# Kernel tuning notes

Hardware: AMD Instinct MI355X
Metric: run time of the kernel (lower is better)

Reference implementation:

```python
import jax, jax.numpy as jnp
import numpy as np

N, D, H = 4096, 1024, 8
DH = D // H
EPS = 1e-5


def layer_norm(x, g, b):
    mu = jnp.mean(x, axis=-1, keepdims=True)
    var = jnp.mean(jnp.square(x - mu), axis=-1, keepdims=True)
    return (x - mu) * jax.lax.rsqrt(var + EPS) * g + b


def setup_inputs() -> dict:
    key = jax.random.key(0)
    ks = jax.random.split(key, 12)
    s = 0.02
    inp = {
        "x": jax.random.normal(ks[0], (N, D), dtype=jnp.float32),
        "adj": (jax.random.uniform(ks[1], (N, N)) < 0.01).astype(jnp.float32),
        "Wq": jax.random.normal(ks[2], (D, D), dtype=jnp.float32) * s,
        "Wk": jax.random.normal(ks[3], (D, D), dtype=jnp.float32) * s,
        "Wv": jax.random.normal(ks[4], (D, D), dtype=jnp.float32) * s,
        "Wo_w": jax.random.normal(ks[5], (D, D), dtype=jnp.float32) * s,
        "Wo_b": jnp.zeros((D,), dtype=jnp.float32),
        "adj_bias": jnp.full((H,), 1.0, dtype=jnp.float32),
        "ln1_g": jnp.ones((D,), dtype=jnp.float32),
        "ln1_b": jnp.zeros((D,), dtype=jnp.float32),
        "ffn_ln_g": jnp.ones((D,), dtype=jnp.float32),
        "ffn_ln_b": jnp.zeros((D,), dtype=jnp.float32),
        "ffn_w1": jax.random.normal(ks[6], (D, 2 * D), dtype=jnp.float32) * s,
        "ffn_b1": jnp.zeros((2 * D,), dtype=jnp.float32),
        "ffn_w2": jax.random.normal(ks[7], (2 * D, D), dtype=jnp.float32) * s,
        "ffn_b2": jnp.zeros((D,), dtype=jnp.float32),
    }
    return inp


def reference(x, adj, Wq, Wk, Wv, Wo_w, Wo_b, adj_bias, ln1_g, ln1_b,
              ffn_ln_g, ffn_ln_b, ffn_w1, ffn_b1, ffn_w2, ffn_b2):
    scale = DH ** -0.5
    Q = (x @ Wq).reshape(N, H, DH)
    K = (x @ Wk).reshape(N, H, DH)
    V = (x @ Wv).reshape(N, H, DH)
    # attn[i,h,j] = <Q_i, K_j> * scale + beta_h * adj[i,j]
    attn = jnp.einsum('bhd,nhd->bhn', Q, K) * scale
    attn = attn + adj_bias[None, :, None] * adj[:, None, :]
    attn = jax.nn.softmax(attn, axis=-1)  # dropout in eval mode -> identity
    out = jnp.einsum('bhn,nhd->bhd', attn, V).reshape(N, D)
    out = out @ Wo_w + Wo_b
    h = layer_norm(x + out, ln1_g, ln1_b)
    f = layer_norm(h, ffn_ln_g, ffn_ln_b)
    f = jax.nn.gelu(f @ ffn_w1 + ffn_b1, approximate=False) @ ffn_w2 + ffn_b2
    return h + f
```

## Files before the change

### kernel.cpp

```cpp
#include <hip/hip_runtime.h>
#include <hip/hip_bf16.h>
#include <cstdint>
#include <cstddef>

typedef __hip_bfloat16 bf16;
typedef __attribute__((ext_vector_type(8))) short short8;
typedef __attribute__((ext_vector_type(4))) short short4v;
typedef __attribute__((ext_vector_type(4))) float floatx4;
typedef unsigned long long u64;

#define DEVI static __device__ __forceinline__

DEVI void load_lds16(const void* g, void* l) {
  __builtin_amdgcn_global_load_lds((const __attribute__((address_space(1))) unsigned int*)g,
                                   (__attribute__((address_space(3))) unsigned int*)l, 16, 0, 0);
}
DEVI short8 ld8(const bf16* p) { return *(const short8*)p; }
DEVI floatx4 mfma16(short8 a, short8 b, floatx4 c) {
  return __builtin_amdgcn_mfma_f32_16x16x32_bf16(a, b, c, 0, 0, 0);
}
DEVI short bfb(float f) { bf16 h = __float2bfloat16(f); return __builtin_bit_cast(short, h); }
DEVI float fbf(short s) { bf16 h = __builtin_bit_cast(bf16, s); return __bfloat162float(h); }

DEVI void tr_tile(const float* in, bf16* out, int R, int C, int bx, int by) {
  __shared__ float t[32][33];
  int c0 = bx * 32, r0 = by * 32;
  int tx = threadIdx.x & 31, ty = threadIdx.x >> 5;
#pragma unroll
  for (int i = 0; i < 32; i += 8) t[ty + i][tx] = in[(size_t)(r0 + ty + i) * C + c0 + tx];
  __syncthreads();
#pragma unroll
  for (int i = 0; i < 32; i += 8)
    out[(size_t)(c0 + ty + i) * R + r0 + tx] = __float2bfloat16(t[tx][ty + i]);
}

__global__ __launch_bounds__(256)
void prep_all(const float* __restrict__ x, bf16* __restrict__ xb,
              const float* __restrict__ adj, u64* __restrict__ bits,
              const float* Wq, const float* Wk, const float* Wv, const float* Wo,
              const float* W1, const float* W2,
              bf16* Wqkvt, bf16* Wot, bf16* W1t, bf16* W2t) {
  int id = blockIdx.x;
  if (id < 4096) {
    const int row = id, tid = threadIdx.x;
    const int wave = tid >> 6, lane = tid & 63;
    float4 v = ((const float4*)(x + (size_t)row * 1024))[tid];
    bf16* o = xb + (size_t)row * 1024 + tid * 4;
    o[0] = __float2bfloat16(v.x); o[1] = __float2bfloat16(v.y);
    o[2] = __float2bfloat16(v.z); o[3] = __float2bfloat16(v.w);
    const float* arow = adj + (size_t)row * 4096;
#pragma unroll
    for (int it = 0; it < 16; it++) {
      int col = it * 256 + tid;
      u64 m = __ballot(arow[col] != 0.f);
      if (lane == 0) bits[(size_t)row * 64 + it * 4 + wave] = m;
    }
  } else if (id < 8192) {
    int q = id - 4096, w = q >> 10, t = q & 1023;
    const float* in = w == 0 ? Wq : w == 1 ? Wk : w == 2 ? Wv : Wo;
    bf16* out = w == 0 ? Wqkvt : w == 1 ? Wqkvt + 1024ull * 1024
              : w == 2 ? Wqkvt + 2048ull * 1024 : Wot;
    tr_tile(in, out, 1024, 1024, t & 31, t >> 5);
  } else if (id < 10240) {
    int t = id - 8192;
    tr_tile(W1, W1t, 1024, 2048, t & 63, t >> 6);
  } else {
    int t = id - 10240;
    tr_tile(W2, W2t, 2048, 1024, t & 31, t >> 5);
  }
}

__global__ __launch_bounds__(256)
void tr_bf16p(const bf16* __restrict__ in, bf16* __restrict__ out, int inLd) {
  __shared__ bf16 t[32][33];
  int c0 = blockIdx.x * 32, r0 = blockIdx.y * 32;
  int tx = threadIdx.x, ty = threadIdx.y;
#pragma unroll
  for (int i = 0; i < 32; i += 8) t[ty + i][tx] = in[(size_t)(r0 + ty + i) * inLd + c0 + tx];
  __syncthreads();
#pragma unroll
  for (int i = 0; i < 32; i += 8) {
    int k = r0 + tx;
    int pk = (k & ~63) | ((k & 15) << 2) | ((k >> 4) & 3);
    out[(size_t)(c0 + ty + i) * 4096 + pk] = t[tx][ty + i];
  }
}

template <int MODE>
__global__ __launch_bounds__(256)
void gemm_bt(const bf16* __restrict__ A, const bf16* __restrict__ Bt,
             const float* __restrict__ bias, const float* __restrict__ resid,
             float* __restrict__ outF, bf16* __restrict__ outB,
             int M, int Nn, int K) {
  __shared__ alignas(16) bf16 As[3][128 * 32];
  __shared__ alignas(16) bf16 Bs[3][128 * 32];
  const int tid = threadIdx.x;
  const int wave = tid >> 6, lane = tid & 63;
  const int m0 = blockIdx.y * 128, n0 = blockIdx.x * 128;
  const int wr = (wave >> 1) * 64, wc = (wave & 1) * 64;
  const int l15 = lane & 15, qq = lane >> 4;
  const int lr = lane >> 2, l4 = lane & 3;
  const int Kspan = K / gridDim.z;
  const int kbeg = blockIdx.z * Kspan;
  const int T = Kspan >> 5;

  floatx4 acc[4][4];
#pragma unroll
  for (int i = 0; i < 4; i++)
#pragma unroll
    for (int j = 0; j < 4; j++) acc[i][j] = (floatx4)0.f;

  const bf16* gA0 = A + (size_t)(m0 + wave * 16 + lr) * K + kbeg + l4 * 8;
  const bf16* gA1 = gA0 + (size_t)64 * K;
  const bf16* gB0 = Bt + (size_t)(n0 + wave * 16 + lr) * K + kbeg + l4 * 8;
  const bf16* gB1 = gB0 + (size_t)64 * K;
  const int lo = wave * 16 * 32;

  auto stage = [&](int t, int buf) {
    int kt = t * 32;
    load_lds16(gA0 + kt, &As[buf][lo]);
    load_lds16(gA1 + kt, &As[buf][64 * 32 + lo]);
    load_lds16(gB0 + kt, &Bs[buf][lo]);
    load_lds16(gB1 + kt, &Bs[buf][64 * 32 + lo]);
  };
  stage(0, 0);
  stage(1, 1);

  int bc = 0;
  for (int t = 0; t < T; ++t) {
    if (t < T - 1) asm volatile("s_waitcnt vmcnt(4) lgkmcnt(0)" ::: "memory");
    else           asm volatile("s_waitcnt vmcnt(0) lgkmcnt(0)" ::: "memory");
    __builtin_amdgcn_s_barrier();
    if (t + 2 < T) { int bs = bc == 0 ? 2 : bc - 1; stage(t + 2, bs); }

    short8 af[4], bfr[4];
#pragma unroll
    for (int mi = 0; mi < 4; mi++) af[mi] = ld8(&As[bc][(wr + mi * 16 + l15) * 32 + qq * 8]);
#pragma unroll
    for (int ni = 0; ni < 4; ni++) bfr[ni] = ld8(&Bs[bc][(wc + ni * 16 + l15) * 32 + qq * 8]);
#pragma unroll
    for (int mi = 0; mi < 4; mi++)
#pragma unroll
      for (int ni = 0; ni < 4; ni++)
        acc[mi][ni] = mfma16(af[mi], bfr[ni], acc[mi][ni]);
    bc = bc == 2 ? 0 : bc + 1;
  }

  const size_t zoff = (size_t)blockIdx.z * M * Nn;
#pragma unroll
  for (int mi = 0; mi < 4; mi++) {
    int row = m0 + wr + mi * 16 + qq * 4;
#pragma unroll
    for (int ni = 0; ni < 4; ni++) {
      int col = n0 + wc + ni * 16 + l15;
      float bv = 0.f;
      if (MODE == 2) bv = bias[col];
      if (MODE == 4 && blockIdx.z == 0) bv = bias[col];
#pragma unroll
      for (int r = 0; r < 4; r++) {
        float v = acc[mi][ni][r] + bv;
        size_t off = (size_t)(row + r) * Nn + col;
        if (MODE == 0) {
          outB[off] = __float2bfloat16(v);
        } else if (MODE == 2) {
          outB[off] = __float2bfloat16(0.5f * v * (1.f + erff(v * 0.70710678118654752f)));
        } else {
          if (resid && blockIdx.z == 1) v += resid[off];
          outF[zoff + off] = v;
        }
      }
    }
  }
}

__global__ __launch_bounds__(256, 2)
void attn_kernel(const bf16* __restrict__ QKV, const bf16* __restrict__ Vtp,
                 const u64* __restrict__ adjbits, const float* __restrict__ adj_bias,
                 bf16* __restrict__ AOpart, float* __restrict__ lpart) {
  __shared__ alignas(16) bf16 Kf[16 * 512];
  __shared__ alignas(16) bf16 Vf[16 * 512];
  __shared__ alignas(16) bf16 Ps[4][32 * 68];
  __shared__ u64 Abits[128 * 16];
  const int q0 = blockIdx.x * 128;
  const int h = blockIdx.y;
  const int split = blockIdx.z;
  const int k0 = split * 1024;
  const int tid = threadIdx.x, wave = tid >> 6, lane = tid & 63;
  const int l15 = lane & 15, qq = lane >> 4;
  const float beta = adj_bias[h];
  const float scale = 0.08838834764831845f;

#pragma unroll
  for (int i = 0; i < 8; i++) {
    int idx = tid + i * 256;
    Abits[idx] = adjbits[(size_t)(q0 + (idx >> 4)) * 64 + split * 16 + (idx & 15)];
  }

  short8 qf[2][4];
#pragma unroll
  for (int mi = 0; mi < 2; mi++)
#pragma unroll
    for (int kk = 0; kk < 4; kk++)
      qf[mi][kk] = ld8(&QKV[(size_t)(q0 + wave * 32 + mi * 16 + l15) * 3072 +
                            h * 128 + kk * 32 + qq * 8]);

  floatx4 o[2][8];
#pragma unroll
  for (int mi = 0; mi < 2; mi++)
#pragma unroll
    for (int ni = 0; ni < 8; ni++) o[mi][ni] = (floatx4)0.f;
  float lrow[2][4];
#pragma unroll
  for (int mi = 0; mi < 2; mi++)
#pragma unroll
    for (int r = 0; r < 4; r++) lrow[mi][r] = 0.f;

  bf16* PsW = &Ps[wave][0];

  auto fetchK = [&](int kt, short8 (&dst)[4]) {
#pragma unroll
    for (int i = 0; i < 4; i++) {
      int fi = wave * 4 + i, ni = fi >> 2, kk = fi & 3;
      dst[i] = ld8(&QKV[(size_t)(kt + ni * 16 + l15) * 3072 + 1024 +
                        h * 128 + kk * 32 + qq * 8]);
    }
  };
  auto fetchV = [&](int kt, short8 (&dst)[4]) {
#pragma unroll
    for (int i = 0; i < 4; i++) {
      int fi = wave * 4 + i, ni = fi >> 1, kk = fi & 1;
      dst[i] = ld8(&Vtp[(size_t)(h * 128 + ni * 16 + l15) * 4096 + kt + kk * 32 + qq * 8]);
    }
  };

  auto iter = [&](int t, short8 (&kc)[4], short8 (&vc)[4]) {
    const int kt = k0 + t * 64;
    __syncthreads();
#pragma unroll
    for (int i = 0; i < 4; i++) {
      *(short8*)&Kf[(wave * 4 + i) * 512 + lane * 8] = kc[i];
      *(short8*)&Vf[(wave * 4 + i) * 512 + lane * 8] = vc[i];
    }
    __syncthreads();
    if (t + 2 < 16) { fetchK(kt + 128, kc); fetchV(kt + 128, vc); }

    floatx4 s[2][4];
#pragma unroll
    for (int mi = 0; mi < 2; mi++)
#pragma unroll
      for (int ni = 0; ni < 4; ni++) s[mi][ni] = (floatx4)0.f;
#pragma unroll
    for (int kk = 0; kk < 4; kk++) {
#pragma unroll
      for (int ni = 0; ni < 4; ni++) {
        short8 kf = ld8(&Kf[(ni * 4 + kk) * 512 + lane * 8]);
        s[0][ni] = mfma16(qf[0][kk], kf, s[0][ni]);
        s[1][ni] = mfma16(qf[1][kk], kf, s[1][ni]);
      }
    }

#pragma unroll
    for (int mi = 0; mi < 2; mi++) {
#pragma unroll
      for (int r = 0; r < 4; r++) {
        int rloc = wave * 32 + mi * 16 + qq * 4 + r;
        u64 bits = Abits[rloc * 16 + t];
        unsigned lo = (unsigned)(bits >> l15);
        unsigned hi = (unsigned)(bits >> (l15 + 32));
        float b0 = (lo & 1u) ? beta : 0.f;
        float b1 = (lo & 0x10000u) ? beta : 0.f;
        float b2 = (hi & 1u) ? beta : 0.f;
        float b3 = (hi & 0x10000u) ? beta : 0.f;
        float p0 = __expf(fmaf(s[mi][0][r], scale, b0));
        float p1 = __expf(fmaf(s[mi][1][r], scale, b1));
        float p2 = __expf(fmaf(s[mi][2][r], scale, b2));
        float p3 = __expf(fmaf(s[mi][3][r], scale, b3));
        lrow[mi][r] += (p0 + p1) + (p2 + p3);
        short4v pk;
        pk.x = bfb(p0); pk.y = bfb(p1); pk.z = bfb(p2); pk.w = bfb(p3);
        *(short4v*)&PsW[(mi * 16 + qq * 4 + r) * 68 + l15 * 4] = pk;
      }
    }

#pragma unroll
    for (int kk = 0; kk < 2; kk++) {
      short8 af0 = ld8(&PsW[(0 + l15) * 68 + kk * 32 + qq * 8]);
      short8 af1 = ld8(&PsW[(16 + l15) * 68 + kk * 32 + qq * 8]);
#pragma unroll
      for (int ni = 0; ni < 8; ni++) {
        short8 vf = ld8(&Vf[(ni * 2 + kk) * 512 + lane * 8]);
        o[0][ni] = mfma16(af0, vf, o[0][ni]);
        o[1][ni] = mfma16(af1, vf, o[1][ni]);
      }
    }
  };

  short8 kpre0[4], vpre0[4], kpre1[4], vpre1[4];
  fetchK(k0, kpre0);       fetchV(k0, vpre0);
  fetchK(k0 + 64, kpre1);  fetchV(k0 + 64, vpre1);

  for (int tt = 0; tt < 8; tt++) {
    iter(2 * tt, kpre0, vpre0);
    iter(2 * tt + 1, kpre1, vpre1);
  }

#pragma unroll
  for (int mi = 0; mi < 2; mi++) {
#pragma unroll
    for (int r = 0; r < 4; r++) {
      float v = lrow[mi][r];
#pragma unroll
      for (int ofs = 1; ofs < 16; ofs <<= 1) v += __shfl_xor(v, ofs, 16);
      int rloc = wave * 32 + mi * 16 + qq * 4 + r;
      int grow = q0 + rloc;
      if (l15 == 0) lpart[((size_t)split * 4096 + grow) * 8 + h] = v;
      bf16* dst = AOpart + ((size_t)split * 4096 + grow) * 1024 + h * 128;
#pragma unroll
      for (int ni = 0; ni < 8; ni++) dst[ni * 16 + l15] = __float2bfloat16(o[mi][ni][r]);
    }
  }
}

__global__ __launch_bounds__(256)
void attn_norm(const bf16* __restrict__ AOpart, const float* __restrict__ lpart,
               bf16* __restrict__ AO) {
  int row = blockIdx.x, tid = threadIdx.x;
  int h = tid >> 5;
  float ls = 0.f;
#pragma unroll
  for (int s = 0; s < 4; s++) ls += lpart[((size_t)s * 4096 + row) * 8 + h];
  float a0 = 0.f, a1 = 0.f, a2 = 0.f, a3 = 0.f;
#pragma unroll
  for (int s = 0; s < 4; s++) {
    short4v v = *(const short4v*)&AOpart[((size_t)s * 4096 + row) * 1024 + tid * 4];
    a0 += fbf(v.x); a1 += fbf(v.y); a2 += fbf(v.z); a3 += fbf(v.w);
  }
  float inv = 1.f / ls;
  bf16* op = AO + (size_t)row * 1024 + tid * 4;
  op[0] = __float2bfloat16(a0 * inv);
  op[1] = __float2bfloat16(a1 * inv);
  op[2] = __float2bfloat16(a2 * inv);
  op[3] = __float2bfloat16(a3 * inv);
}

DEVI void block_sum2(float& a, float& b, float* red) {
#pragma unroll
  for (int o = 1; o < 64; o <<= 1) { a += __shfl_xor(a, o, 64); b += __shfl_xor(b, o, 64); }
  int wv = threadIdx.x >> 6;
  if ((threadIdx.x & 63) == 0) { red[wv] = a; red[4 + wv] = b; }
  __syncthreads();
  a = red[0] + red[1] + red[2] + red[3];
  b = red[4] + red[5] + red[6] + red[7];
  __syncthreads();
}

__global__ __launch_bounds__(256)
void ln2_kernel(const float* __restrict__ x, const float* __restrict__ ao0,
                const float* __restrict__ ao1,
                const float* __restrict__ g1, const float* __restrict__ b1,
                const float* __restrict__ g2, const float* __restrict__ b2,
                float* __restrict__ hout, bf16* __restrict__ fln) {
  __shared__ float red[8];
  const int row = blockIdx.x, tid = threadIdx.x;
  float4 xv = ((const float4*)(x + (size_t)row * 1024))[tid];
  float4 av = ((const float4*)(ao0 + (size_t)row * 1024))[tid];
  float4 aw = ((const float4*)(ao1 + (size_t)row * 1024))[tid];
  float s0 = xv.x + av.x + aw.x, s1 = xv.y + av.y + aw.y;
  float s2 = xv.z + av.z + aw.z, s3 = xv.w + av.w + aw.w;
  float sum = s0 + s1 + s2 + s3;
  float ssq = s0 * s0 + s1 * s1 + s2 * s2 + s3 * s3;
  block_sum2(sum, ssq, red);
  float mu = sum * (1.f / 1024.f);
  float rs = rsqrtf(ssq * (1.f / 1024.f) - mu * mu + 1e-5f);
  float4 gv = ((const float4*)g1)[tid], bv = ((const float4*)b1)[tid];
  float h0 = (s0 - mu) * rs * gv.x + bv.x;
  float h1 = (s1 - mu) * rs * gv.y + bv.y;
  float h2 = (s2 - mu) * rs * gv.z + bv.z;
  float h3 = (s3 - mu) * rs * gv.w + bv.w;
  float4 hv; hv.x = h0; hv.y = h1; hv.z = h2; hv.w = h3;
  ((float4*)(hout + (size_t)row * 1024))[tid] = hv;
  float sum2 = h0 + h1 + h2 + h3;
  float ssq2 = h0 * h0 + h1 * h1 + h2 * h2 + h3 * h3;
  block_sum2(sum2, ssq2, red);
  float mu2 = sum2 * (1.f / 1024.f);
  float rs2 = rsqrtf(ssq2 * (1.f / 1024.f) - mu2 * mu2 + 1e-5f);
  float4 g2v = ((const float4*)g2)[tid], b2v = ((const float4*)b2)[tid];
  bf16* op = fln + (size_t)row * 1024 + tid * 4;
  op[0] = __float2bfloat16((h0 - mu2) * rs2 * g2v.x + b2v.x);
  op[1] = __float2bfloat16((h1 - mu2) * rs2 * g2v.y + b2v.y);
  op[2] = __float2bfloat16((h2 - mu2) * rs2 * g2v.z + b2v.z);
  op[3] = __float2bfloat16((h3 - mu2) * rs2 * g2v.w + b2v.w);
}

__global__ __launch_bounds__(256)
void add2_kernel(const float* __restrict__ a, const float* __restrict__ b,
                 float* __restrict__ o) {
  int i = blockIdx.x * 256 + threadIdx.x;
  float4 va = ((const float4*)a)[i];
  float4 vb = ((const float4*)b)[i];
  float4 vo; vo.x = va.x + vb.x; vo.y = va.y + vb.y;
  vo.z = va.z + vb.z; vo.w = va.w + vb.w;
  ((float4*)o)[i] = vo;
}

extern "C" void kernel_launch(void* const* d_in, const int* in_sizes, int n_in,
                              void* d_out, int out_size, void* d_ws, size_t ws_size,
                              hipStream_t stream) {
  const float* x    = (const float*)d_in[0];
  const float* adj  = (const float*)d_in[1];
  const float* Wq   = (const float*)d_in[2];
  const float* Wk   = (const float*)d_in[3];
  const float* Wv   = (const float*)d_in[4];
  const float* Wo   = (const float*)d_in[5];
  const float* Wob  = (const float*)d_in[6];
  const float* adjb = (const float*)d_in[7];
  const float* g1   = (const float*)d_in[8];
  const float* b1   = (const float*)d_in[9];
  const float* g2   = (const float*)d_in[10];
  const float* b2   = (const float*)d_in[11];
  const float* W1   = (const float*)d_in[12];
  const float* fb1  = (const float*)d_in[13];
  const float* W2   = (const float*)d_in[14];
  const float* fb2  = (const float*)d_in[15];
  float* out = (float*)d_out;

  char* w = (char*)d_ws;
  size_t off = 0;
  auto take = [&](size_t bytes) {
    char* p = w + off;
    off += (bytes + 255) & ~(size_t)255;
    return p;
  };
  bf16* xb    = (bf16*)take(4096ull * 1024 * 2);
  bf16* Wqkvt = (bf16*)take(3072ull * 1024 * 2);
  bf16* Wot   = (bf16*)take(1024ull * 1024 * 2);
  bf16* W1t   = (bf16*)take(2048ull * 1024 * 2);
  bf16* W2t   = (bf16*)take(1024ull * 2048 * 2);
  bf16* QKV   = (bf16*)take(4096ull * 3072 * 2);
  bf16* Vtp   = (bf16*)take(1024ull * 4096 * 2);
  bf16* AO    = (bf16*)take(4096ull * 1024 * 2);
  u64*  adjbits = (u64*)take(4096ull * 64 * 8);
  float* lpart  = (float*)take(4ull * 4096 * 8 * 4);
  char* big = take(32ull << 20);
  bf16*  AOpart = (bf16*)big;
  float* WoP    = (float*)big;
  float* F2P    = (float*)big;
  float* H   = (float*)take(4096ull * 1024 * 4);
  bf16*  FLN = (bf16*)take(4096ull * 1024 * 2);
  bf16*  G   = (bf16*)take(4096ull * 2048 * 2);

  dim3 tb(32, 8);
  prep_all<<<12288, 256, 0, stream>>>(x, xb, adj, adjbits, Wq, Wk, Wv, Wo, W1, W2,
                                      Wqkvt, Wot, W1t, W2t);
  gemm_bt<0><<<dim3(24, 32, 1), 256, 0, stream>>>(xb, Wqkvt, nullptr, nullptr,
                                                  nullptr, QKV, 4096, 3072, 1024);
  tr_bf16p<<<dim3(32, 128), tb, 0, stream>>>(QKV + 2048, Vtp, 3072);
  attn_kernel<<<dim3(32, 8, 4), 256, 0, stream>>>(QKV, Vtp, adjbits, adjb, AOpart, lpart);
  attn_norm<<<4096, 256, 0, stream>>>(AOpart, lpart, AO);
  gemm_bt<4><<<dim3(8, 32, 2), 256, 0, stream>>>(AO, Wot, Wob, nullptr,
                                                 WoP, nullptr, 4096, 1024, 1024);
  ln2_kernel<<<4096, 256, 0, stream>>>(x, WoP, WoP + 4096ull * 1024, g1, b1, g2, b2, H, FLN);
  gemm_bt<2><<<dim3(16, 32, 1), 256, 0, stream>>>(FLN, W1t, fb1, nullptr,
                                                  nullptr, G, 4096, 2048, 1024);
  gemm_bt<4><<<dim3(8, 32, 2), 256, 0, stream>>>(G, W2t, fb2, H,
                                                 F2P, nullptr, 4096, 1024, 2048);
  add2_kernel<<<4096, 256, 0, stream>>>(F2P, F2P + 4096ull * 1024, out);
}
```

Baseline: 472.7 us.

## Prefetch adjacency bits into registers and shrink K/V prefetch depth to one tile

```diff
diff --git a/kernel.cpp b/kernel.cpp
--- a/kernel.cpp
+++ b/kernel.cpp
@@ -180,7 +180,6 @@
   __shared__ alignas(16) bf16 Kf[16 * 512];
   __shared__ alignas(16) bf16 Vf[16 * 512];
   __shared__ alignas(16) bf16 Ps[4][32 * 68];
-  __shared__ u64 Abits[128 * 16];
   const int q0 = blockIdx.x * 128;
   const int h = blockIdx.y;
   const int split = blockIdx.z;
@@ -190,12 +189,6 @@
   const float beta = adj_bias[h];
   const float scale = 0.08838834764831845f;
 
-#pragma unroll
-  for (int i = 0; i < 8; i++) {
-    int idx = tid + i * 256;
-    Abits[idx] = adjbits[(size_t)(q0 + (idx >> 4)) * 64 + split * 16 + (idx & 15)];
-  }
-
   short8 qf[2][4];
 #pragma unroll
   for (int mi = 0; mi < 2; mi++)
@@ -217,6 +210,8 @@
 
   bf16* PsW = &Ps[wave][0];
 
+  short8 kpre[4], vpre[4];
+  u64 abc[2][4], abn[2][4];
   auto fetchK = [&](int kt, short8 (&dst)[4]) {
 #pragma unroll
     for (int i = 0; i < 4; i++) {
@@ -232,17 +227,28 @@
       dst[i] = ld8(&Vtp[(size_t)(h * 128 + ni * 16 + l15) * 4096 + kt + kk * 32 + qq * 8]);
     }
   };
-
-  auto iter = [&](int t, short8 (&kc)[4], short8 (&vc)[4]) {
+  auto fetchA = [&](int t, u64 (&ab)[2][4]) {
+#pragma unroll
+    for (int mi = 0; mi < 2; mi++)
+#pragma unroll
+      for (int r = 0; r < 4; r++)
+        ab[mi][r] = adjbits[(size_t)(q0 + wave * 32 + mi * 16 + qq * 4 + r) * 64 +
+                            split * 16 + t];
+  };
+  fetchK(k0, kpre);
+  fetchV(k0, vpre);
+  fetchA(0, abc);
+
+  for (int t = 0; t < 16; t++) {
     const int kt = k0 + t * 64;
     __syncthreads();
 #pragma unroll
     for (int i = 0; i < 4; i++) {
-      *(short8*)&Kf[(wave * 4 + i) * 512 + lane * 8] = kc[i];
-      *(short8*)&Vf[(wave * 4 + i) * 512 + lane * 8] = vc[i];
+      *(short8*)&Kf[(wave * 4 + i) * 512 + lane * 8] = kpre[i];
+      *(short8*)&Vf[(wave * 4 + i) * 512 + lane * 8] = vpre[i];
     }
     __syncthreads();
-    if (t + 2 < 16) { fetchK(kt + 128, kc); fetchV(kt + 128, vc); }
+    if (t < 15) { fetchK(kt + 64, kpre); fetchV(kt + 64, vpre); fetchA(t + 1, abn); }
 
     floatx4 s[2][4];
 #pragma unroll
@@ -263,8 +269,7 @@
     for (int mi = 0; mi < 2; mi++) {
 #pragma unroll
       for (int r = 0; r < 4; r++) {
-        int rloc = wave * 32 + mi * 16 + qq * 4 + r;
-        u64 bits = Abits[rloc * 16 + t];
+        u64 bits = abc[mi][r];
         unsigned lo = (unsigned)(bits >> l15);
         unsigned hi = (unsigned)(bits >> (l15 + 32));
         float b0 = (lo & 1u) ? beta : 0.f;
@@ -293,15 +298,10 @@
         o[1][ni] = mfma16(af1, vf, o[1][ni]);
       }
     }
-  };
-
-  short8 kpre0[4], vpre0[4], kpre1[4], vpre1[4];
-  fetchK(k0, kpre0);       fetchV(k0, vpre0);
-  fetchK(k0 + 64, kpre1);  fetchV(k0 + 64, vpre1);
-
-  for (int tt = 0; tt < 8; tt++) {
-    iter(2 * tt, kpre0, vpre0);
-    iter(2 * tt + 1, kpre1, vpre1);
+#pragma unroll
+    for (int mi = 0; mi < 2; mi++)
+#pragma unroll
+      for (int r = 0; r < 4; r++) abc[mi][r] = abn[mi][r];
   }
 
 #pragma unroll
```

Result: faster. 459.9 us (-2.7%).
